# Kernel optimization log

Measured on AMD Instinct MI355X. Metric: run time of the kernel, lower is better.

## Reference

```python
import jax, jax.numpy as jnp
import numpy as np

B, L, D = 8, 2048, 256
D_MODEL = 1024
NUM_SIGNALS = 16
MAX_POSITIONS = 4096
ROLE_OUTPUT = 2  # role id used for the CLS token


def setup_inputs() -> dict:
    key = jax.random.key(0)
    ks = jax.random.split(key, 12)
    emb = jax.random.normal(ks[0], (B, L, D), dtype=jnp.float32)
    pos = jax.random.randint(ks[1], (B, L), 1, MAX_POSITIONS + 1)          # pos >= 1 for real tokens
    sid = jax.random.randint(ks[2], (B, L), 0, NUM_SIGNALS)
    role = jax.random.randint(ks[3], (B, L), 0, 3)
    padding_mask = jax.random.uniform(ks[4], (B, L)) < 0.75                # True = real token
    # learned parameters
    proj_W = jax.random.normal(ks[5], (NUM_SIGNALS, D_MODEL, D), dtype=jnp.float32) * (1.0 / np.sqrt(D))
    proj_b = jax.random.normal(ks[6], (NUM_SIGNALS, D_MODEL), dtype=jnp.float32) * 0.01
    cls_content = jax.random.normal(ks[7], (D_MODEL,), dtype=jnp.float32)
    pos_embed = jax.random.normal(ks[8], (MAX_POSITIONS + 1, D_MODEL), dtype=jnp.float32)
    id_embed = jax.random.normal(ks[9], (NUM_SIGNALS + 1, D_MODEL), dtype=jnp.float32)
    role_embed = jax.random.normal(ks[10], (3, D_MODEL), dtype=jnp.float32)
    return dict(emb=emb, pos=pos, sid=sid, role=role, padding_mask=padding_mask,
                proj_W=proj_W, proj_b=proj_b, cls_content=cls_content,
                pos_embed=pos_embed, id_embed=id_embed, role_embed=role_embed)


def reference(emb, pos, sid, role, padding_mask,
              proj_W, proj_b, cls_content, pos_embed, id_embed, role_embed):
    Bv, Lv, _ = emb.shape
    S, d_model, _ = proj_W.shape
    cls_id = S

    # Grouped per-signal projection: one GEMM per signal id, select per token.
    tokens = jnp.zeros((Bv, Lv, d_model), dtype=emb.dtype)
    for s in range(S):
        proj_s = jnp.einsum('bld,ed->ble', emb, proj_W[s]) + proj_b[s]   # (B, L, d_model)
        keep = ((sid == s) & padding_mask)[..., None]
        tokens = jnp.where(keep, proj_s, tokens)

    # Prepend CLS
    cls = jnp.broadcast_to(cls_content[None, None, :], (Bv, 1, d_model))
    tokens = jnp.concatenate([cls, tokens], axis=1)                       # (B, L+1, d_model)

    pos_full = jnp.concatenate([jnp.zeros((Bv, 1), dtype=pos.dtype), pos], axis=1)
    sid_full = jnp.concatenate([jnp.full((Bv, 1), cls_id, dtype=sid.dtype), sid], axis=1)
    role_full = jnp.concatenate([jnp.full((Bv, 1), ROLE_OUTPUT, dtype=role.dtype), role], axis=1)

    tokens = tokens + pos_embed[pos_full] + id_embed[sid_full] + role_embed[role_full]

    attn_keep = jnp.concatenate([jnp.ones((Bv, 1), dtype=bool), padding_mask], axis=1)
    return tokens, attn_keep
```

## Files before the change

### kernel.cpp

```cpp
#include <hip/hip_runtime.h>
#include <hip/hip_bf16.h>
#include <stdint.h>

#define B_ 8
#define L_ 2048
#define NTOK 16384
#define DK 256
#define DM 1024
#define NS 16
#define LOUT 2049
#define TOK_OUT (B_*LOUT*DM)
#define ATTN_OUT (B_*LOUT)
#define PCAP 2048
#define UCAP 8192

typedef unsigned short u16;
typedef unsigned int u32;
typedef __bf16 bf16x8 __attribute__((ext_vector_type(8)));
typedef float f32x4 __attribute__((ext_vector_type(4)));

__device__ inline u32 packbf2(float lo, float hi) {
    u32 a, b;
    __builtin_memcpy(&a, &lo, 4);
    __builtin_memcpy(&b, &hi, 4);
    a = (a + 0x8000u) >> 16;
    b = (b + 0x8000u) & 0xFFFF0000u;
    return a | b;
}

__device__ inline void gll16(const void* g, void* l) {
    __builtin_amdgcn_global_load_lds(
        (const __attribute__((address_space(1))) unsigned int*)g,
        (__attribute__((address_space(3))) unsigned int*)l, 16, 0, 0);
}

#define WS_CUR 0
#define WS_UCUR 16
#define WS_WIDTH 32
#define WS_PERM 64
#define WS_UNM (64 + NS * PCAP)
#define EMB_OFF 262144ULL
#define W_OFF (EMB_OFF + 16384ULL * 512ULL)
#define WS_NEED (W_OFF + 16384ULL * 512ULL)

__device__ inline int sniff_width(const unsigned char* mb, int tid, int* sh) {
    if (tid == 0) { sh[0] = 0; sh[1] = 0; sh[2] = 0; }
    __syncthreads();
    int c1ge2 = 0, ge2 = 0, oddnz = 0;
    const u32* mw = (const u32*)mb;
    #pragma unroll
    for (int i = 0; i < 16; i++) {
        u32 x = mw[tid * 16 + i];
        u32 b0 = x & 0xFF, b1 = (x >> 8) & 0xFF, b2 = (x >> 16) & 0xFF, b3 = x >> 24;
        if (b1 >= 2) c1ge2 = 1;
        if (b0 >= 2 || b1 >= 2 || b2 >= 2 || b3 >= 2) ge2 = 1;
        if ((b1 | b3) != 0) oddnz = 1;
    }
    if (c1ge2) atomicOr(&sh[0], 1);
    if (ge2) atomicOr(&sh[1], 1);
    if (oddnz) atomicOr(&sh[2], 1);
    __syncthreads();
    if (sh[0]) return 2;
    if (sh[1]) return 4;
    if (sh[2]) return 1;
    return 4;
}

__device__ inline int decode_mask(const unsigned char* mb, int t, int width) {
    if (width == 1) return mb[t] != 0;
    if (width == 2) return ((const u16*)mb)[t] != 0;
    return ((const u32*)mb)[t] != 0;
}

#define SORT_B 64
#define PREP_GRID (SORT_B + 1024)

__global__ __launch_bounds__(256) void prep_all(
    const unsigned char* __restrict__ mb, const int* __restrict__ sid,
    const float* __restrict__ emb, const float* __restrict__ W,
    int* __restrict__ wsi, unsigned char* __restrict__ wsb) {
    __shared__ int sh[3];
    __shared__ int lcnt[NS], gbase[NS];
    __shared__ int lcnt_u, gbase_u;
    int bid = blockIdx.x;
    int tid = threadIdx.x;
    int lane = tid & 63;
    int wv = tid >> 6;

    if (bid < SORT_B) {
        if (tid < NS) lcnt[tid] = 0;
        if (tid == 0) lcnt_u = 0;
        int width = sniff_width(mb, tid, sh);
        if (bid == 0 && tid == 0) wsi[WS_WIDTH] = width;
        int t = bid * 256 + tid;
        int m = decode_mask(mb, t, width);
        int s = sid[t];
        int lr;
        if (m) lr = atomicAdd(&lcnt[s], 1);
        else   lr = atomicAdd(&lcnt_u, 1);
        __syncthreads();
        if (tid < NS) gbase[tid] = atomicAdd(&wsi[WS_CUR + tid], lcnt[tid]);
        if (tid == 0) gbase_u = atomicAdd(&wsi[WS_UCUR], lcnt_u);
        __syncthreads();
        if (m) {
            int r = gbase[s] + lr;
            if (r < PCAP) wsi[WS_PERM + s * PCAP + r] = t;
        } else {
            int r = gbase_u + lr;
            if (r < UCAP) wsi[WS_UNM + r] = t;
        }
        return;
    }

    int cb = bid - SORT_B;
    const float* src;
    u16* dst;
    if (cb < 512) {
        src = emb;
        dst = (u16*)(wsb + EMB_OFF);
    } else {
        cb -= 512;
        src = W;
        dst = (u16*)(wsb + W_OFF);
    }
    int r0 = cb * 32 + wv * 8;
    #pragma unroll 4
    for (int i = 0; i < 8; i++) {
        int r = r0 + i;
        float4 a = *(const float4*)(src + (size_t)r * DK + lane * 4);
        uint2 o;
        o.x = packbf2(a.x, a.y);
        o.y = packbf2(a.z, a.w);
        *(uint2*)(dst + (size_t)r * DK + lane * 4) = o;
    }
}

#define GG 4608
#define CLS_B0 (GG - 67)
#define ATTN_B0 (GG - 65)
#define EPAD 68

__global__ __launch_bounds__(256, 8) void gemm_big(
    const unsigned char* __restrict__ mb,
    const int* __restrict__ pos, const int* __restrict__ sid,
    const int* __restrict__ role,
    const float* __restrict__ bias, const float* __restrict__ cls,
    const float* __restrict__ pos_emb, const float* __restrict__ id_emb,
    const float* __restrict__ role_emb,
    const int* __restrict__ wsi, const unsigned char* __restrict__ wsb,
    float* __restrict__ out) {
    __shared__ unsigned char smem[64 * EPAD * 4];
    __shared__ int toks[64];
    u16 (*As)[64 * 32] = (u16(*)[64 * 32])smem;
    u16 (*Bs)[64 * 32] = (u16(*)[64 * 32])(smem + 8192);
    float* etile = (float*)smem;
    int bi = (int)blockIdx.x;
    int tid = threadIdx.x;
    int lane = tid & 63;
    int wv = tid >> 6;

    int cnts[NS];
    int mtot = 0;
    #pragma unroll
    for (int i = 0; i < NS; i++) {
        int c = wsi[WS_CUR + i];
        cnts[i] = c > PCAP ? PCAP : c;
        mtot += (cnts[i] + 63) >> 6;
    }
    int xcd = bi & 7;
    int j = bi >> 3;
    int m_lo = (xcd * mtot) >> 3;
    int m_hi = ((xcd + 1) * mtot) >> 3;
    int cm = m_hi - m_lo;
    bool doGemm = (cm > 0 && j < cm * 16);
    int s = -1, lrt = 0, n0 = 0;
    if (doGemm) {
        int nt = j / cm;
        int m = m_lo + (j - nt * cm);
        n0 = nt << 6;
        #pragma unroll
        for (int i = 0; i < NS; i++) {
            int rt = (cnts[i] + 63) >> 6;
            if (s < 0) {
                if (m < rt) { s = i; lrt = m; }
                else m -= rt;
            }
        }
        if (s < 0) doGemm = false;
    }

    if (doGemm) {
        int rowsValid = cnts[s] - lrt * 64;
        if (rowsValid > 64) rowsValid = 64;

        if (tid < 64) {
            int base = WS_PERM + s * PCAP + lrt * 64;
            toks[tid] = wsi[base + ((tid < rowsValid) ? tid : 0)];
        }
        __syncthreads();

        const u16* Eb = (const u16*)(wsb + EMB_OFF);
        const u16* Bb = (const u16*)(wsb + W_OFF) + (size_t)(s * DM + n0) * DK;

        int srow = lane >> 2;
        int slseg = lane & 3;
        int arow = wv * 16 + srow;
        int ags = (slseg - (arow >> 1)) & 3;
        const u16* Asrc = Eb + (size_t)toks[arow] * DK;

        f32x4 acc[4];
        #pragma unroll
        for (int jn = 0; jn < 4; jn++) acc[jn] = (f32x4){0.f, 0.f, 0.f, 0.f};

        int mcol = lane & 15;
        int quad = lane >> 4;

#define STAGE(kc, bf)                                                          \
        {                                                                      \
            gll16(Asrc + (kc) * 32 + ags * 8, &As[bf][(wv * 16) * 32]);        \
            gll16(Bb + (size_t)arow * DK + (kc) * 32 + ags * 8,                \
                  &Bs[bf][(wv * 16) * 32]);                                    \
        }

        STAGE(0, 0)
        #pragma unroll
        for (int kc = 0; kc < 8; ++kc) {
            __syncthreads();
            if (kc < 7) STAGE(kc + 1, (kc + 1) & 1)
            int bf = kc & 1;
            bf16x8 af, bfr[4];
            {
                int row = wv * 16 + mcol;
                int sg = (quad + (row >> 1)) & 3;
                af = *(const bf16x8*)(&As[bf][row * 32 + sg * 8]);
            }
            #pragma unroll
            for (int jn = 0; jn < 4; jn++) {
                int row = jn * 16 + mcol;
                int sg = (quad + (row >> 1)) & 3;
                bfr[jn] = *(const bf16x8*)(&Bs[bf][row * 32 + sg * 8]);
            }
            #pragma unroll
            for (int jn = 0; jn < 4; jn++)
                acc[jn] = __builtin_amdgcn_mfma_f32_16x16x32_bf16(
                    af, bfr[jn], acc[jn], 0, 0, 0);
        }
#undef STAGE

        int ecol = (lane & 15) * 4;
        int rp = lane >> 4;
        f32x4 bc4 = *(const f32x4*)(bias + (size_t)s * DM + n0 + ecol);
        f32x4 ic4 = *(const f32x4*)(id_emb + (size_t)s * DM + n0 + ecol);
        f32x4 bi4 = bc4 + ic4;

        __syncthreads();
        #pragma unroll
        for (int jn = 0; jn < 4; jn++) {
            #pragma unroll
            for (int r = 0; r < 4; r++) {
                int er = wv * 16 + quad * 4 + r;
                etile[er * EPAD + jn * 16 + mcol] = acc[jn][r];
            }
        }
        #pragma unroll
        for (int p = 0; p < 4; p++) {
            int er = wv * 16 + p * 4 + rp;
            if (er < rowsValid) {
                int t = toks[er];
                int pz = pos[t];
                int ro = role[t];
                int b = t >> 11, l = t & 2047;
                size_t orow = (size_t)(b * LOUT + l + 1) * DM + n0 + ecol;
                f32x4 av = *(const f32x4*)&etile[er * EPAD + ecol];
                f32x4 pv = *(const f32x4*)(pos_emb + (size_t)pz * DM + n0 + ecol);
                f32x4 rv = *(const f32x4*)(role_emb + (size_t)ro * DM + n0 + ecol);
                f32x4 o = av + bi4 + pv + rv;
                __builtin_nontemporal_store(o, (f32x4*)(out + orow));
            }
        }
    }

    {
        int ucnt = wsi[WS_UCUR];
        if (ucnt > UCAP) ucnt = UCAP;
        for (int idx = (GG - 1 - bi) * 4 + wv; idx < ucnt; idx += GG * 4) {
            int t = wsi[WS_UNM + idx];
            int p = pos[t], sd = sid[t], ro = role[t];
            int b = t >> 11, l = t & 2047;
            size_t orow = (size_t)(b * LOUT + l + 1) * DM;
            const float* pr = pos_emb + (size_t)p * DM;
            const float* ir = id_emb + (size_t)sd * DM;
            const float* rr = role_emb + (size_t)ro * DM;
            #pragma unroll
            for (int it = 0; it < 4; it++) {
                int c = it * 256 + lane * 4;
                f32x4 a = *(const f32x4*)(pr + c);
                f32x4 d = *(const f32x4*)(ir + c);
                f32x4 e = *(const f32x4*)(rr + c);
                f32x4 o = a + d + e;
                __builtin_nontemporal_store(o, (f32x4*)(out + orow + c));
            }
        }
        if (bi >= CLS_B0 && bi < ATTN_B0) {
            int b = (bi - CLS_B0) * 4 + wv;
            size_t orow = (size_t)(b * LOUT) * DM;
            #pragma unroll
            for (int it = 0; it < 4; it++) {
                int c = it * 256 + lane * 4;
                f32x4 cc = *(const f32x4*)(cls + c);
                f32x4 a = *(const f32x4*)(pos_emb + c);
                f32x4 d = *(const f32x4*)(id_emb + NS * DM + c);
                f32x4 e = *(const f32x4*)(role_emb + 2 * DM + c);
                f32x4 o = cc + a + d + e;
                *(f32x4*)(out + orow + c) = o;
            }
        }
        if (bi >= ATTN_B0) {
            int width = wsi[WS_WIDTH];
            int i = (bi - ATTN_B0) * 256 + tid;
            if (i < ATTN_OUT) {
                int b = i / LOUT;
                int jj = i - b * LOUT;
                float val = (jj == 0) ? 1.0f
                    : (float)decode_mask(mb, b * L_ + jj - 1, width);
                out[TOK_OUT + i] = val;
            }
        }
    }
}

extern "C" void kernel_launch(void* const* d_in, const int* in_sizes, int n_in,
                              void* d_out, int out_size, void* d_ws, size_t ws_size,
                              hipStream_t stream) {
    const float* emb = (const float*)d_in[0];
    const int* pos = (const int*)d_in[1];
    const int* sid = (const int*)d_in[2];
    const int* role = (const int*)d_in[3];
    const unsigned char* mask = (const unsigned char*)d_in[4];
    const float* W = (const float*)d_in[5];
    const float* bias = (const float*)d_in[6];
    const float* cls = (const float*)d_in[7];
    const float* pos_emb = (const float*)d_in[8];
    const float* id_emb = (const float*)d_in[9];
    const float* role_emb = (const float*)d_in[10];
    float* out = (float*)d_out;
    int* wsi = (int*)d_ws;
    unsigned char* wsb = (unsigned char*)d_ws;

    (void)hipMemsetAsync(wsi, 0, 64 * sizeof(int), stream);
    hipLaunchKernelGGL(prep_all, dim3(PREP_GRID), dim3(256), 0, stream,
                       mask, sid, emb, W, wsi, wsb);
    hipLaunchKernelGGL(gemm_big, dim3(GG), dim3(256), 0, stream,
                       mask, pos, sid, role, bias, cls, pos_emb, id_emb,
                       role_emb, wsi, wsb, out);
}
```

Measured before the change: 155.4 us.

## Retile grouped GEMM to 32-row x full-width tiles with 512-thread blocks

```diff
diff --git a/kernel.cpp b/kernel.cpp
--- a/kernel.cpp
+++ b/kernel.cpp
@@ -135,12 +135,12 @@
     }
 }
 
-#define GG 4608
-#define CLS_B0 (GG - 67)
-#define ATTN_B0 (GG - 65)
-#define EPAD 68
-
-__global__ __launch_bounds__(256, 8) void gemm_big(
+#define GG 640
+#define CLS_B0 (GG - 34)
+#define ATTN_B0 (GG - 33)
+#define ESTR 1032
+
+__global__ __launch_bounds__(512, 4) void gemm_big(
     const unsigned char* __restrict__ mb,
     const int* __restrict__ pos, const int* __restrict__ sid,
     const int* __restrict__ role,
@@ -149,10 +149,10 @@
     const float* __restrict__ role_emb,
     const int* __restrict__ wsi, const unsigned char* __restrict__ wsb,
     float* __restrict__ out) {
-    __shared__ unsigned char smem[64 * EPAD * 4];
-    __shared__ int toks[64];
-    u16 (*As)[64 * 32] = (u16(*)[64 * 32])smem;
-    u16 (*Bs)[64 * 32] = (u16(*)[64 * 32])(smem + 8192);
+    __shared__ unsigned char smem[67584];
+    __shared__ int toks[32];
+    u16* Bs = (u16*)smem;
+    u16* As = (u16*)(smem + 65536);
     float* etile = (float*)smem;
     int bi = (int)blockIdx.x;
     int tid = threadIdx.x;
@@ -165,22 +165,20 @@
     for (int i = 0; i < NS; i++) {
         int c = wsi[WS_CUR + i];
         cnts[i] = c > PCAP ? PCAP : c;
-        mtot += (cnts[i] + 63) >> 6;
+        mtot += (cnts[i] + 31) >> 5;
     }
     int xcd = bi & 7;
     int j = bi >> 3;
     int m_lo = (xcd * mtot) >> 3;
     int m_hi = ((xcd + 1) * mtot) >> 3;
     int cm = m_hi - m_lo;
-    bool doGemm = (cm > 0 && j < cm * 16);
-    int s = -1, lrt = 0, n0 = 0;
+    bool doGemm = (cm > 0 && j < cm);
+    int s = -1, lrt = 0;
     if (doGemm) {
-        int nt = j / cm;
-        int m = m_lo + (j - nt * cm);
-        n0 = nt << 6;
+        int m = m_lo + j;
         #pragma unroll
         for (int i = 0; i < NS; i++) {
-            int rt = (cnts[i] + 63) >> 6;
+            int rt = (cnts[i] + 31) >> 5;
             if (s < 0) {
                 if (m < rt) { s = i; lrt = m; }
                 else m -= rt;
@@ -190,100 +188,122 @@
     }
 
     if (doGemm) {
-        int rowsValid = cnts[s] - lrt * 64;
-        if (rowsValid > 64) rowsValid = 64;
-
-        if (tid < 64) {
-            int base = WS_PERM + s * PCAP + lrt * 64;
+        int rowsValid = cnts[s] - lrt * 32;
+        if (rowsValid > 32) rowsValid = 32;
+
+        if (tid < 32) {
+            int base = WS_PERM + s * PCAP + lrt * 32;
             toks[tid] = wsi[base + ((tid < rowsValid) ? tid : 0)];
         }
         __syncthreads();
 
         const u16* Eb = (const u16*)(wsb + EMB_OFF);
-        const u16* Bb = (const u16*)(wsb + W_OFF) + (size_t)(s * DM + n0) * DK;
-
-        int srow = lane >> 2;
-        int slseg = lane & 3;
-        int arow = wv * 16 + srow;
-        int ags = (slseg - (arow >> 1)) & 3;
-        const u16* Asrc = Eb + (size_t)toks[arow] * DK;
-
-        f32x4 acc[4];
-        #pragma unroll
-        for (int jn = 0; jn < 4; jn++) acc[jn] = (f32x4){0.f, 0.f, 0.f, 0.f};
+        const u16* Bb = (const u16*)(wsb + W_OFF) + (size_t)(s * DM) * DK;
+
+        const u16* Asrc = Eb;
+        if (wv < 2) {
+            int arow = wv * 16 + (lane >> 2);
+            Asrc = Eb + (size_t)toks[arow] * DK;
+        }
+        int sseg = lane & 3;
+
+        f32x4 acc[16];
+        #pragma unroll
+        for (int jn = 0; jn < 16; jn++) acc[jn] = (f32x4){0.f, 0.f, 0.f, 0.f};
 
         int mcol = lane & 15;
         int quad = lane >> 4;
-
-#define STAGE(kc, bf)                                                          \
+        int rw = wv & 1;
+        int cw = wv >> 1;
+
+        int arow_r = rw * 16 + mcol;
+        int asl = (quad + (arow_r >> 1)) & 3;
+
+#define STAGE(kc)                                                              \
         {                                                                      \
-            gll16(Asrc + (kc) * 32 + ags * 8, &As[bf][(wv * 16) * 32]);        \
-            gll16(Bb + (size_t)arow * DK + (kc) * 32 + ags * 8,                \
-                  &Bs[bf][(wv * 16) * 32]);                                    \
-        }
-
-        STAGE(0, 0)
+            _Pragma("unroll")                                                  \
+            for (int i = 0; i < 8; i++) {                                      \
+                int brow = wv * 128 + i * 16 + (lane >> 2);                    \
+                int gseg = (sseg - (brow >> 1)) & 3;                           \
+                gll16(Bb + (size_t)brow * DK + (kc) * 32 + gseg * 8,           \
+                      &Bs[(wv * 128 + i * 16) * 32]);                          \
+            }                                                                  \
+            if (wv < 2) {                                                      \
+                int arow = wv * 16 + (lane >> 2);                              \
+                int gseg = (sseg - (arow >> 1)) & 3;                           \
+                gll16(Asrc + (kc) * 32 + gseg * 8, &As[(wv * 16) * 32]);       \
+            }                                                                  \
+        }
+
         #pragma unroll
         for (int kc = 0; kc < 8; ++kc) {
+            STAGE(kc)
             __syncthreads();
-            if (kc < 7) STAGE(kc + 1, (kc + 1) & 1)
-            int bf = kc & 1;
-            bf16x8 af, bfr[4];
-            {
-                int row = wv * 16 + mcol;
-                int sg = (quad + (row >> 1)) & 3;
-                af = *(const bf16x8*)(&As[bf][row * 32 + sg * 8]);
-            }
+            bf16x8 af = *(const bf16x8*)&As[arow_r * 32 + asl * 8];
             #pragma unroll
-            for (int jn = 0; jn < 4; jn++) {
-                int row = jn * 16 + mcol;
-                int sg = (quad + (row >> 1)) & 3;
-                bfr[jn] = *(const bf16x8*)(&Bs[bf][row * 32 + sg * 8]);
-            }
+            for (int jn = 0; jn < 16; jn++) {
+                int brow_r = cw * 256 + jn * 16 + mcol;
+                int bsl = (quad + (brow_r >> 1)) & 3;
+                bf16x8 bf_ = *(const bf16x8*)&Bs[brow_r * 32 + bsl * 8];
+                acc[jn] = __builtin_amdgcn_mfma_f32_16x16x32_bf16(
+                    af, bf_, acc[jn], 0, 0, 0);
+            }
+            __syncthreads();
+        }
+#undef STAGE
+
+        f32x4 bi4[4];
+        #pragma unroll
+        for (int c = 0; c < 4; c++) {
+            int col = c * 256 + lane * 4;
+            f32x4 bv = *(const f32x4*)(bias + (size_t)s * DM + col);
+            f32x4 iv = *(const f32x4*)(id_emb + (size_t)s * DM + col);
+            bi4[c] = bv + iv;
+        }
+
+        #pragma unroll
+        for (int h = 0; h < 2; h++) {
+            if (rw == h) {
+                #pragma unroll
+                for (int jn = 0; jn < 16; jn++) {
+                    int col = cw * 256 + jn * 16 + mcol;
+                    #pragma unroll
+                    for (int r = 0; r < 4; r++)
+                        etile[(quad * 4 + r) * ESTR + col] = acc[jn][r];
+                }
+            }
+            __syncthreads();
             #pragma unroll
-            for (int jn = 0; jn < 4; jn++)
-                acc[jn] = __builtin_amdgcn_mfma_f32_16x16x32_bf16(
-                    af, bfr[jn], acc[jn], 0, 0, 0);
-        }
-#undef STAGE
-
-        int ecol = (lane & 15) * 4;
-        int rp = lane >> 4;
-        f32x4 bc4 = *(const f32x4*)(bias + (size_t)s * DM + n0 + ecol);
-        f32x4 ic4 = *(const f32x4*)(id_emb + (size_t)s * DM + n0 + ecol);
-        f32x4 bi4 = bc4 + ic4;
-
-        __syncthreads();
-        #pragma unroll
-        for (int jn = 0; jn < 4; jn++) {
-            #pragma unroll
-            for (int r = 0; r < 4; r++) {
-                int er = wv * 16 + quad * 4 + r;
-                etile[er * EPAD + jn * 16 + mcol] = acc[jn][r];
-            }
-        }
-        #pragma unroll
-        for (int p = 0; p < 4; p++) {
-            int er = wv * 16 + p * 4 + rp;
-            if (er < rowsValid) {
-                int t = toks[er];
-                int pz = pos[t];
-                int ro = role[t];
-                int b = t >> 11, l = t & 2047;
-                size_t orow = (size_t)(b * LOUT + l + 1) * DM + n0 + ecol;
-                f32x4 av = *(const f32x4*)&etile[er * EPAD + ecol];
-                f32x4 pv = *(const f32x4*)(pos_emb + (size_t)pz * DM + n0 + ecol);
-                f32x4 rv = *(const f32x4*)(role_emb + (size_t)ro * DM + n0 + ecol);
-                f32x4 o = av + bi4 + pv + rv;
-                __builtin_nontemporal_store(o, (f32x4*)(out + orow));
-            }
+            for (int rr = 0; rr < 2; rr++) {
+                int er = wv * 2 + rr;
+                int rowT = h * 16 + er;
+                if (rowT < rowsValid) {
+                    int t = toks[rowT];
+                    int pz = pos[t];
+                    int ro = role[t];
+                    int b = t >> 11, l = t & 2047;
+                    size_t orow = (size_t)(b * LOUT + l + 1) * DM;
+                    const float* prow = pos_emb + (size_t)pz * DM;
+                    const float* rrow = role_emb + (size_t)ro * DM;
+                    #pragma unroll
+                    for (int c = 0; c < 4; c++) {
+                        int col = c * 256 + lane * 4;
+                        f32x4 av = *(const f32x4*)&etile[er * ESTR + col];
+                        f32x4 pv = *(const f32x4*)(prow + col);
+                        f32x4 rv = *(const f32x4*)(rrow + col);
+                        f32x4 o = av + bi4[c] + pv + rv;
+                        __builtin_nontemporal_store(o, (f32x4*)(out + orow + col));
+                    }
+                }
+            }
+            __syncthreads();
         }
     }
 
     {
         int ucnt = wsi[WS_UCUR];
         if (ucnt > UCAP) ucnt = UCAP;
-        for (int idx = (GG - 1 - bi) * 4 + wv; idx < ucnt; idx += GG * 4) {
+        for (int idx = (GG - 1 - bi) * 8 + wv; idx < ucnt; idx += GG * 8) {
             int t = wsi[WS_UNM + idx];
             int p = pos[t], sd = sid[t], ro = role[t];
             int b = t >> 11, l = t & 2047;
@@ -301,8 +321,8 @@
                 __builtin_nontemporal_store(o, (f32x4*)(out + orow + c));
             }
         }
-        if (bi >= CLS_B0 && bi < ATTN_B0) {
-            int b = (bi - CLS_B0) * 4 + wv;
+        if (bi == CLS_B0) {
+            int b = wv;
             size_t orow = (size_t)(b * LOUT) * DM;
             #pragma unroll
             for (int it = 0; it < 4; it++) {
@@ -317,7 +337,7 @@
         }
         if (bi >= ATTN_B0) {
             int width = wsi[WS_WIDTH];
-            int i = (bi - ATTN_B0) * 256 + tid;
+            int i = (bi - ATTN_B0) * 512 + tid;
             if (i < ATTN_OUT) {
                 int b = i / LOUT;
                 int jj = i - b * LOUT;
@@ -350,7 +370,7 @@
     (void)hipMemsetAsync(wsi, 0, 64 * sizeof(int), stream);
     hipLaunchKernelGGL(prep_all, dim3(PREP_GRID), dim3(256), 0, stream,
                        mask, sid, emb, W, wsi, wsb);
-    hipLaunchKernelGGL(gemm_big, dim3(GG), dim3(256), 0, stream,
+    hipLaunchKernelGGL(gemm_big, dim3(GG), dim3(512), 0, stream,
                        mask, pos, sid, role, bias, cls, pos_emb, id_emb,
                        role_emb, wsi, wsb, out);
 }
```

After: 157.7 us. About the same (+1.4%).
